# Kernel optimization log

Measured on AMD Instinct MI355X. Metric: run time of the kernel, lower is better.

## Reference

```python
import jax, jax.numpy as jnp
from jax import lax
import numpy as np

E = 3            # num_experts
HEAD_CONV = 128  # head_conv
N_HEADS = 3      # hm, wh, reg
HEAD_CH = 2      # channels per head
BN_EPS = 1e-5


def _conv(x, w, stride, pad, groups=1):
    return lax.conv_general_dilated(
        x, w, (stride, stride), [(pad, pad), (pad, pad)],
        feature_group_count=groups,
        dimension_numbers=('NCHW', 'OIHW', 'NCHW'))


def _maxpool3s2p1(x):
    return lax.reduce_window(
        x, -jnp.inf, lax.max, (1, 1, 3, 3), (1, 1, 2, 2),
        ((0, 0), (0, 0), (1, 1), (1, 1)))


def setup_inputs() -> dict:
    key = jax.random.key(0)
    ks = jax.random.split(key, 8)
    B, C, T, H, W = 16, 3, 5, 384, 384
    s = 0.05
    inp = {
        'x': jax.random.normal(ks[0], (B, C, T, H, W), jnp.float32),
        # gating network params
        'g_conv_w': jax.random.normal(ks[1], (64, C * T, 7, 7), jnp.float32) * s,
        'g_bn_gamma': jnp.ones((64,), jnp.float32),
        'g_bn_beta': jnp.zeros((64,), jnp.float32),
        'g_bn_mean': jnp.zeros((64,), jnp.float32),
        'g_bn_var': jnp.ones((64,), jnp.float32),
        'g_fc_w': jax.random.normal(ks[2], (E, 64), jnp.float32) * s,
        'g_fc_b': jnp.zeros((E,), jnp.float32),
        # frozen expert params (stacked over expert dim E)
        'e_conv1_w': jax.random.normal(ks[3], (E, 64, C * T, 7, 7), jnp.float32) * s,
        'e_conv1_b': jnp.zeros((E, 64), jnp.float32),
        'e_head_w1': jax.random.normal(ks[4], (E, N_HEADS * HEAD_CONV, 64, 3, 3), jnp.float32) * s,
        'e_head_b1': jnp.zeros((E, N_HEADS * HEAD_CONV), jnp.float32),
        'e_head_w2': jax.random.normal(ks[5], (E, N_HEADS * HEAD_CH, HEAD_CONV, 1, 1), jnp.float32) * s,
        'e_head_b2': jnp.zeros((E, N_HEADS * HEAD_CH), jnp.float32),
    }
    return inp


def reference(x, g_conv_w, g_bn_gamma, g_bn_beta, g_bn_mean, g_bn_var,
              g_fc_w, g_fc_b, e_conv1_w, e_conv1_b,
              e_head_w1, e_head_b1, e_head_w2, e_head_b2):
    b, c, t, h, w = x.shape
    xr = x.reshape(b, c * t, h, w)

    # ---- ConvGatingNetwork ----
    f = _conv(xr, g_conv_w, 2, 3)                                  # [B,64,H/2,W/2]
    inv = g_bn_gamma / jnp.sqrt(g_bn_var + BN_EPS)
    f = f * inv[None, :, None, None] + (g_bn_beta - g_bn_mean * inv)[None, :, None, None]
    f = jax.nn.relu(f)
    f = _maxpool3s2p1(f)                                           # [B,64,H/4,W/4]
    feat = f.mean(axis=(2, 3))                                     # [B,64]
    logits = feat @ g_fc_w.T + g_fc_b                              # [B,E]
    idx = jnp.argmax(logits, axis=1)                               # top-1
    onehot = jax.nn.one_hot(idx, E, dtype=logits.dtype)            # [B,E]
    density = onehot.mean(axis=0)
    density_proxy = jax.nn.softmax(logits, axis=1).mean(axis=0)
    aux_loss = (density * density_proxy).sum() * E

    # ---- Experts (frozen DSFNet stand-in), computed densely then gathered ----
    def expert(cw, cb, hw1, hb1, hw2, hb2):
        y = jax.nn.relu(_conv(xr, cw, 4, 3) + cb[None, :, None, None])       # [B,64,H/4,W/4]
        y = jax.nn.relu(_conv(y, hw1, 1, 1) + hb1[None, :, None, None])      # [B,384,h,w]
        y = _conv(y, hw2, 1, 0, groups=N_HEADS) + hb2[None, :, None, None]   # [B,6,h,w]
        return y

    out_all = jax.vmap(expert)(e_conv1_w, e_conv1_b, e_head_w1, e_head_b1,
                               e_head_w2, e_head_b2)               # [E,B,6,h,w]
    out_all = lax.stop_gradient(out_all)  # experts frozen + torch.no_grad
    out = jnp.einsum('be,ebchw->bchw', onehot, out_all)            # per-sample top-1 gather
    return out, 0.01 * aux_loss
```

## Files before the change

### kernel.cpp

```cpp
#include <hip/hip_runtime.h>
#include <math.h>

#define BB 16
#define CIN 15
#define HW 384
#define XPL 147456
#define NX 35389440
#define PH 96
#define GW 192
#define YP 98
#define Y1IPL (98*98*64)
#define OUT_ELEMS (BB*6*PH*PH)

#define OFF_WG   0
#define OFF_WE1  122880
#define OFF_WH   491520
#define OFF_GSH  1818624
#define OFF_FEAT 1818880
#define OFF_IDX  1822976
#define OFF_CBUF 2097152

typedef __attribute__((ext_vector_type(8))) short short8;
typedef __attribute__((ext_vector_type(4))) float floatx4;
typedef __attribute__((ext_vector_type(4))) unsigned int uintx4;
typedef __attribute__((ext_vector_type(2))) unsigned int uintx2;

__device__ __forceinline__ unsigned bf16rne(float f) {
  unsigned u = __float_as_uint(f);
  unsigned r = ((u >> 16) & 1u) + 0x7FFFu;
  return (u + r) >> 16;
}
__device__ __forceinline__ float bf2f(unsigned short s) {
  return __uint_as_float(((unsigned)s) << 16);
}

__global__ __launch_bounds__(256) void k_prep(
    const float* __restrict__ g_conv_w, const float* __restrict__ e_conv1_w,
    const float* __restrict__ e_head_w1,
    const float* __restrict__ gamma, const float* __restrict__ var,
    const float* __restrict__ beta,  const float* __restrict__ mean,
    unsigned char* __restrict__ wsb)
{
  int i = blockIdx.x * 256 + threadIdx.x;
  unsigned short* Wg  = (unsigned short*)(wsb + OFF_WG);
  unsigned short* We1 = (unsigned short*)(wsb + OFF_WE1);
  unsigned short* Wh  = (unsigned short*)(wsb + OFF_WH);
  float* gsh = (float*)(wsb + OFF_GSH);
  if (i < 61440) {
    int j = i & 7, lane = (i >> 3) & 63, mtc = i >> 9;
    int mt = mtc & 3, c = mtc >> 2, ic = c >> 1, h = c & 1;
    int oc = mt * 16 + (lane & 15), q = lane >> 4;
    int ky = 4 * h + q, kx = j;
    float v = 0.f;
    if (ky < 7 && kx < 7) v = g_conv_w[oc * 735 + ic * 49 + ky * 7 + kx];
    float inv = gamma[oc] * rsqrtf(var[oc] + 1e-5f);
    Wg[i] = (unsigned short)bf16rne(v * inv);
  } else if (i < 245760) {
    int r = i - 61440;
    int e = r / 61440, r2 = r % 61440;
    int j = r2 & 7, lane = (r2 >> 3) & 63, mtc = r2 >> 9;
    int mt = mtc & 3, c = mtc >> 2, ic = c >> 1, h = c & 1;
    int oc = mt * 16 + (lane & 15), q = lane >> 4;
    int ky = 4 * h + q, kx = j;
    float v = 0.f;
    if (ky < 7 && kx < 7) v = e_conv1_w[(e * 64 + oc) * 735 + ic * 49 + ky * 7 + kx];
    We1[r] = (unsigned short)bf16rne(v);
  } else if (i < 909312) {
    int r = i - 245760;
    int e = r / 221184, r2 = r % 221184;
    int j = r2 & 7, lane = (r2 >> 3) & 63, mtc = r2 >> 9;
    int mt = mtc % 24, chunk = mtc / 24;
    int kk = chunk >> 1, ih = chunk & 1;
    int oc = mt * 16 + (lane & 15), q = lane >> 4;
    int ic = ih * 32 + q * 8 + j;
    Wh[r] = (unsigned short)bf16rne(e_head_w1[((e * 384 + oc) * 64 + ic) * 9 + kk]);
  } else if (i < 909376) {
    int oc = i - 909312;
    float inv = gamma[oc] * rsqrtf(var[oc] + 1e-5f);
    gsh[oc] = beta[oc] - mean[oc] * inv;
  }
}

__global__ __launch_bounds__(256, 3) void k_gconv(
    const float* __restrict__ x, const unsigned short* __restrict__ Wg,
    const float* __restrict__ gsh, unsigned short* __restrict__ Cbuf)
{
  const int t = threadIdx.x, w = t >> 6, lane = t & 63, q = lane >> 4, ln = lane & 15;

  int lin = blockIdx.x + 12 * (blockIdx.y + 12 * blockIdx.z);
  int nl = (lin & 7) * 288 + (lin >> 3);
  const int b = nl / 144; int r144 = nl - b * 144;
  const int by = r144 / 12, bx = r144 - by * 12;

  const int px0 = bx * 16, py0 = by * 16;
  const int iy0 = 2 * py0 - 3, ix0 = 2 * px0 - 3;
  const bool edge = (bx == 0) | (bx == 11) | (by == 0) | (by == 11);
  const int xbase = b * CIN * XPL;

  __shared__ unsigned tilU[2][2280];

  const bool act = (t < 228);
  const int lic = t / 76, r2 = t - lic * 76, srow = r2 >> 1, half = r2 & 1;
  const int iy = iy0 + srow;
  const int A = ix0 + 20 * half - 1;
  const unsigned rowm = (iy >= 0 && iy < HW) ? 0xFFFFFFFFu : 0u;
  const int abase = xbase + iy * HW + A;
  const int dloc = (lic * 38 + srow) * 20 + 10 * half;

  floatx4 F[6];

  auto issue = [&](int c) {
    if (!act) return;
    int a = abase + (c * 3 + lic) * XPL;
    if (!edge) {
      const float* src = x + a;
#pragma unroll
      for (int s = 0; s < 6; ++s) F[s] = *(const floatx4*)(src + 4 * s);
    } else {
#pragma unroll
      for (int s = 0; s < 6; ++s) {
        int as = a + 4 * s;
        as = max(as, 0); as = min(as, NX - 4);
        F[s] = *(const floatx4*)(x + as);
      }
    }
  };

  auto commit = [&](unsigned* buf) {
    if (!act) return;
    float f[24];
#pragma unroll
    for (int s = 0; s < 6; ++s) {
      f[4*s] = F[s].x; f[4*s+1] = F[s].y; f[4*s+2] = F[s].z; f[4*s+3] = F[s].w;
    }
    unsigned* dst = buf + dloc;
    if (!edge) {
#pragma unroll
      for (int jj = 0; jj < 5; ++jj) {
        uintx2 pr;
        pr.x = bf16rne(f[1 + 4*jj]) | (bf16rne(f[2 + 4*jj]) << 16);
        pr.y = bf16rne(f[3 + 4*jj]) | (bf16rne(f[4 + 4*jj]) << 16);
        *(uintx2*)(dst + 2 * jj) = pr;
      }
    } else {
#pragma unroll
      for (int jj = 0; jj < 5; ++jj) {
        uintx2 pr;
#pragma unroll
        for (int k = 0; k < 2; ++k) {
          int j = 2 * jj + k;
          int cc = A + 1 + 2 * j;
          unsigned m = rowm;
          m &= ((cc >= 0) && (cc < HW)) ? 0xFFFFFFFFu : 0xFFFF0000u;
          m &= ((cc + 1 >= 0) && (cc + 1 < HW)) ? 0xFFFFFFFFu : 0x0000FFFFu;
          unsigned d = (bf16rne(f[1 + 2*j]) | (bf16rne(f[2 + 2*j]) << 16)) & m;
          if (k == 0) pr.x = d; else pr.y = d;
        }
        *(uintx2*)(dst + 2 * jj) = pr;
      }
    }
  };

  floatx4 acc[4][4];
#pragma unroll
  for (int mt = 0; mt < 4; ++mt)
#pragma unroll
    for (int nt = 0; nt < 4; ++nt) acc[mt][nt] = 0.f;

  issue(0);
  commit(tilU[0]);
  __syncthreads();

#pragma unroll 1
  for (int c = 0; c < 5; ++c) {
    if (c < 4) issue(c + 1);
    const unsigned* buf = tilU[c & 1];
#pragma unroll
    for (int l2 = 0; l2 < 3; ++l2) {
      const int ic = c * 3 + l2;
#pragma unroll
      for (int h = 0; h < 2; ++h) {
        short8 af[4];
#pragma unroll
        for (int mt = 0; mt < 4; ++mt)
          af[mt] = *(const short8*)(Wg + (((ic * 2 + h) * 4 + mt) << 9) + lane * 8);
        short8 bfv[4];
#pragma unroll
        for (int nt = 0; nt < 4; ++nt) {
          int rrow = 2 * (w * 4 + nt) + 4 * h + q;
          int bd = l2 * 760 + rrow * 20 + ln;
          union { unsigned u[4]; short8 s; } cv;
          cv.u[0] = buf[bd]; cv.u[1] = buf[bd + 1];
          cv.u[2] = buf[bd + 2]; cv.u[3] = buf[bd + 3];
          bfv[nt] = cv.s;
        }
#pragma unroll
        for (int mt = 0; mt < 4; ++mt)
#pragma unroll
          for (int nt = 0; nt < 4; ++nt)
            acc[mt][nt] = __builtin_amdgcn_mfma_f32_16x16x32_bf16(af[mt], bfv[nt], acc[mt][nt], 0, 0, 0);
      }
    }
    if (c < 4) commit(tilU[(c + 1) & 1]);
    __syncthreads();
  }

#pragma unroll
  for (int nt = 0; nt < 4; ++nt) {
    int py = py0 + w * 4 + nt, px = px0 + ln;
    size_t rowo = (((size_t)b * GW + py) * GW + px) * 64;
#pragma unroll
    for (int mt = 0; mt < 4; ++mt) {
      int ocb = mt * 16 + q * 4;
      float v0 = fmaxf(acc[mt][nt][0] + gsh[ocb + 0], 0.f);
      float v1 = fmaxf(acc[mt][nt][1] + gsh[ocb + 1], 0.f);
      float v2 = fmaxf(acc[mt][nt][2] + gsh[ocb + 2], 0.f);
      float v3 = fmaxf(acc[mt][nt][3] + gsh[ocb + 3], 0.f);
      uintx2 pr;
      pr.x = (bf16rne(v1) << 16) | bf16rne(v0);
      pr.y = (bf16rne(v3) << 16) | bf16rne(v2);
      *(uintx2*)(Cbuf + rowo + ocb) = pr;
    }
  }
}

__global__ __launch_bounds__(256) void k_pool(const unsigned short* __restrict__ Cb,
                                              float* __restrict__ feat)
{
  const int py = blockIdx.x, b = blockIdx.y;
  const int t = threadIdx.x, oc = t & 63, strip = t >> 6;
  const unsigned short* base = Cb + (size_t)b * GW * GW * 64 + oc;
  float sum = 0.f;
  for (int px = strip * 24; px < strip * 24 + 24; ++px) {
    float m = 0.f;
#pragma unroll
    for (int dy = 0; dy < 3; ++dy) {
      int row = 2 * py - 1 + dy;
      if (row < 0 || row >= GW) continue;
#pragma unroll
      for (int dx = 0; dx < 3; ++dx) {
        int col = 2 * px - 1 + dx;
        if (col < 0 || col >= GW) continue;
        m = fmaxf(m, bf2f(base[((size_t)row * GW + col) * 64]));
      }
    }
    sum += m;
  }
  __shared__ float red[4][64];
  red[strip][oc] = sum;
  __syncthreads();
  if (t < 64) {
    float s = red[0][oc] + red[1][oc] + red[2][oc] + red[3][oc];
    atomicAdd(&feat[b * 64 + oc], s);
  }
}

__global__ __launch_bounds__(64) void k_gate_fc(
    const float* __restrict__ feat, const float* __restrict__ fcw,
    const float* __restrict__ fcb, int* __restrict__ idxb,
    float* __restrict__ out_aux)
{
  __shared__ float sm[16][3];
  __shared__ int sidx[16];
  int t = threadIdx.x;
  if (t < 16) {
    float l[3];
#pragma unroll
    for (int e = 0; e < 3; ++e) {
      float s = fcb[e];
      for (int c = 0; c < 64; ++c)
        s = fmaf(feat[t * 64 + c] * (1.f / 9216.f), fcw[e * 64 + c], s);
      l[e] = s;
    }
    int best = 0; float bv = l[0];
    if (l[1] > bv) { bv = l[1]; best = 1; }
    if (l[2] > bv) { bv = l[2]; best = 2; }
    sidx[t] = best; idxb[t] = best;
    float mx = fmaxf(l[0], fmaxf(l[1], l[2]));
    float e0 = expf(l[0] - mx), e1 = expf(l[1] - mx), e2 = expf(l[2] - mx);
    float d = e0 + e1 + e2;
    sm[t][0] = e0 / d; sm[t][1] = e1 / d; sm[t][2] = e2 / d;
  }
  __syncthreads();
  if (t == 0) {
    float aux = 0.f;
    for (int e = 0; e < 3; ++e) {
      float cnt = 0.f, pr = 0.f;
      for (int b = 0; b < 16; ++b) { cnt += (sidx[b] == e) ? 1.f : 0.f; pr += sm[b][e]; }
      aux += (cnt / 16.f) * (pr / 16.f);
    }
    *out_aux = 0.01f * aux * 3.f;
  }
}

__global__ __launch_bounds__(256) void k_zring(unsigned short* __restrict__ Y1)
{
  const int b = blockIdx.x, t = threadIdx.x;
  uintx4* Yv = (uintx4*)Y1;
  uintx4 z = 0;
  for (int i = t; i < 3104; i += 256) {
    int v;
    if (i < 784) {
      v = (b * YP + 0) * 784 + i;
    } else if (i < 1568) {
      v = (b * YP + 97) * 784 + (i - 784);
    } else {
      int j = i - 1568;
      int colg = j / 768;
      int jj = j - colg * 768;
      int col = colg ? 97 : 0;
      int rr = 1 + (jj >> 3);
      v = (b * YP + rr) * 784 + col * 8 + (jj & 7);
    }
    Yv[v] = z;
  }
}

__global__ __launch_bounds__(256, 4) void k_econv(
    const float* __restrict__ x, const unsigned short* __restrict__ We1,
    const float* __restrict__ biasp, const int* __restrict__ idxb,
    unsigned short* __restrict__ Y1)
{
  const int t = threadIdx.x, w = t >> 6, lane = t & 63, q = lane >> 4, ln = lane & 15;
  const int b = blockIdx.z;
  const int e = idxb[b];
  const unsigned short* W = We1 + e * 61440;
  const float* bs = biasp + e * 64;
  const int px0 = blockIdx.x * 16, py0 = blockIdx.y * 8;
  const int px = px0 + ln;

  const int c0 = 4 * px - 3;
  const int acol = c0 - 1;
  unsigned pm[4];
#pragma unroll
  for (int j = 0; j < 4; ++j) {
    int t0 = 2 * j, t1 = 2 * j + 1;
    unsigned m0 = (c0 + t0 >= 0 && c0 + t0 < HW) ? 0x0000FFFFu : 0u;
    unsigned m1 = (c0 + t1 >= 0 && c0 + t1 < HW) ? 0xFFFF0000u : 0u;
    pm[j] = m0 | m1;
  }

  int syq[2];
#pragma unroll
  for (int nt = 0; nt < 2; ++nt) syq[nt] = 4 * (py0 + w * 2 + nt) + q - 3;
  const int xbase = b * CIN * XPL;

  floatx4 acc[4][2];
#pragma unroll
  for (int mt = 0; mt < 4; ++mt)
#pragma unroll
    for (int nt = 0; nt < 2; ++nt) acc[mt][nt] = 0.f;

#pragma unroll 3
  for (int ic = 0; ic < CIN; ++ic) {
    const int icb = xbase + ic * XPL;
#pragma unroll
    for (int h = 0; h < 2; ++h) {
      short8 af[4];
#pragma unroll
      for (int mt = 0; mt < 4; ++mt)
        af[mt] = *(const short8*)(W + (((ic * 2 + h) * 4 + mt) << 9) + lane * 8);
      short8 bf[2];
#pragma unroll
      for (int nt = 0; nt < 2; ++nt) {
        int iy = syq[nt] + 4 * h;
        bool rv = (iy >= 0) && (iy < HW) && ((4 * h + q) < 7);
        int a0 = icb + iy * HW + acol;
        a0 = max(a0, 0); a0 = min(a0, NX - 12);
        const float* fp = x + a0;
        floatx4 fA = *(const floatx4*)(fp);
        floatx4 fB = *(const floatx4*)(fp + 4);
        floatx4 fC = *(const floatx4*)(fp + 8);
        float g[8];
        g[0] = fA.y; g[1] = fA.z; g[2] = fA.w; g[3] = fB.x;
        g[4] = fB.y; g[5] = fB.z; g[6] = fB.w; g[7] = fC.x;
        union { unsigned u[4]; short8 s; } cv;
#pragma unroll
        for (int j = 0; j < 4; ++j) {
          unsigned p = __builtin_amdgcn_perm(__float_as_uint(g[2 * j + 1]),
                                             __float_as_uint(g[2 * j]), 0x07060302u);
          p &= pm[j];
          cv.u[j] = rv ? p : 0u;
        }
        bf[nt] = cv.s;
      }
#pragma unroll
      for (int mt = 0; mt < 4; ++mt)
#pragma unroll
        for (int nt = 0; nt < 2; ++nt)
          acc[mt][nt] = __builtin_amdgcn_mfma_f32_16x16x32_bf16(af[mt], bf[nt], acc[mt][nt], 0, 0, 0);
    }
  }

#pragma unroll
  for (int nt = 0; nt < 2; ++nt) {
    int py = py0 + w * 2 + nt;
    size_t rowo = (((size_t)b * YP + py + 1) * YP + px + 1) * 64;
#pragma unroll
    for (int mt = 0; mt < 4; ++mt) {
      int ocb = mt * 16 + q * 4;
      float v0 = fmaxf(acc[mt][nt][0] + bs[ocb + 0], 0.f);
      float v1 = fmaxf(acc[mt][nt][1] + bs[ocb + 1], 0.f);
      float v2 = fmaxf(acc[mt][nt][2] + bs[ocb + 2], 0.f);
      float v3 = fmaxf(acc[mt][nt][3] + bs[ocb + 3], 0.f);
      uintx2 pr;
      pr.x = (bf16rne(v1) << 16) | bf16rne(v0);
      pr.y = (bf16rne(v3) << 16) | bf16rne(v2);
      *(uintx2*)(Y1 + rowo + ocb) = pr;
    }
  }
}

__global__ __launch_bounds__(768, 3) void k_headm(
    const unsigned short* __restrict__ Y1, const unsigned short* __restrict__ Whp,
    const float* __restrict__ b1, const float* __restrict__ w2,
    const float* __restrict__ b2, const int* __restrict__ idxb,
    float* __restrict__ out)
{
  const int t = threadIdx.x, w = t >> 6, lane = t & 63, q = lane >> 4, ln = lane & 15;
  const int wo = w & 3, wn = w >> 2;
  const int b = blockIdx.z, px0 = blockIdx.x * 16, py0 = blockIdx.y * 6;
  const int e = idxb[b];
  const unsigned short* W = Whp + e * 221184;

  __shared__ unsigned short patch[8 * 18 * 72];
  __shared__ float sred[6][4][16][6];

  {
    uintx4 vv[2];
#pragma unroll
    for (int r = 0; r < 2; ++r) {
      int i = r * 768 + t;
      if (i < 1152) {
        int row = i / 144, rem = i % 144, col = rem >> 3, s = rem & 7;
        vv[r] = *(const uintx4*)(Y1 + (((size_t)b * YP + py0 + row) * YP + (px0 + col)) * 64 + s * 8);
      }
    }
#pragma unroll
    for (int r = 0; r < 2; ++r) {
      int i = r * 768 + t;
      if (i < 1152) {
        int row = i / 144, rem = i % 144, col = rem >> 3, s = rem & 7;
        *(uintx4*)(patch + (row * 18 + col) * 72 + s * 8) = vv[r];
      }
    }
  }
  __syncthreads();

  floatx4 acc[6][2];
#pragma unroll
  for (int mt = 0; mt < 6; ++mt)
#pragma unroll
    for (int j = 0; j < 2; ++j) acc[mt][j] = 0.f;

#pragma unroll
  for (int kk = 0; kk < 9; ++kk) {
    const int ky = kk / 3, kx = kk % 3;
#pragma unroll
    for (int ih = 0; ih < 2; ++ih) {
      short8 bf[2];
#pragma unroll
      for (int j = 0; j < 2; ++j) {
        int nt = wn * 2 + j;
        int off = ((nt + ky) * 18 + (ln + kx)) * 72 + ih * 32 + q * 8;
        bf[j] = *(const short8*)(patch + off);
      }
      const int cbase = ((kk * 2 + ih) * 24 + wo * 6) << 9;
#pragma unroll
      for (int mt = 0; mt < 6; ++mt) {
        short8 af = *(const short8*)(W + cbase + (mt << 9) + lane * 8);
#pragma unroll
        for (int j = 0; j < 2; ++j)
          acc[mt][j] = __builtin_amdgcn_mfma_f32_16x16x32_bf16(af, bf[j], acc[mt][j], 0, 0, 0);
      }
    }
  }

#pragma unroll
  for (int j = 0; j < 2; ++j) {
    const int nt = wn * 2 + j;
    float part[6] = {0.f, 0.f, 0.f, 0.f, 0.f, 0.f};
#pragma unroll
    for (int mt = 0; mt < 6; ++mt) {
      int ocb = wo * 96 + mt * 16 + q * 4;
#pragma unroll
      for (int r = 0; r < 4; ++r) {
        int oc = ocb + r;
        float y = fmaxf(acc[mt][j][r] + b1[e * 384 + oc], 0.f);
        int g = oc >> 7, kb = oc & 127;
        part[2 * g]     += y * w2[(e * 6 + 2 * g) * 128 + kb];
        part[2 * g + 1] += y * w2[(e * 6 + 2 * g + 1) * 128 + kb];
      }
    }
#pragma unroll
    for (int c = 0; c < 6; ++c) {
      part[c] += __shfl_down(part[c], 32);
      part[c] += __shfl_down(part[c], 16);
    }
    if (q == 0) {
#pragma unroll
      for (int c = 0; c < 6; ++c) sred[nt][wo][ln][c] = part[c];
    }
  }
  __syncthreads();
  if (t < 576) {
    int pix = t / 6, c = t % 6;
    int nt = pix >> 4, pl = pix & 15;
    float s = sred[nt][0][pl][c] + sred[nt][1][pl][c] + sred[nt][2][pl][c] +
              sred[nt][3][pl][c] + b2[e * 6 + c];
    out[(((size_t)(b * 6 + c)) * PH + (py0 + nt)) * PH + (px0 + pl)] = s;
  }
}

extern "C" void kernel_launch(void* const* d_in, const int* in_sizes, int n_in,
                              void* d_out, int out_size, void* d_ws, size_t ws_size,
                              hipStream_t stream)
{
  const float* x         = (const float*)d_in[0];
  const float* g_fc_w    = (const float*)d_in[6];
  const float* g_fc_b    = (const float*)d_in[7];
  const float* e_conv1_b = (const float*)d_in[9];
  const float* e_head_b1 = (const float*)d_in[11];
  const float* e_head_w2 = (const float*)d_in[12];
  const float* e_head_b2 = (const float*)d_in[13];

  unsigned char* wsb = (unsigned char*)d_ws;
  unsigned short* Wg  = (unsigned short*)(wsb + OFF_WG);
  unsigned short* We1 = (unsigned short*)(wsb + OFF_WE1);
  unsigned short* Wh  = (unsigned short*)(wsb + OFF_WH);
  float* gsh  = (float*)(wsb + OFF_GSH);
  float* feat = (float*)(wsb + OFF_FEAT);
  int*   idxb = (int*)(wsb + OFF_IDX);
  unsigned short* Cbuf = (unsigned short*)(wsb + OFF_CBUF);
  unsigned short* Y1   = (unsigned short*)(wsb + OFF_CBUF);

  float* out = (float*)d_out;
  float* out_aux = out + OUT_ELEMS;

  hipMemsetAsync(feat, 0, 16 * 64 * sizeof(float), stream);
  hipLaunchKernelGGL(k_prep, dim3(3553), dim3(256), 0, stream,
                     (const float*)d_in[1], (const float*)d_in[8], (const float*)d_in[10],
                     (const float*)d_in[2], (const float*)d_in[5],
                     (const float*)d_in[3], (const float*)d_in[4], wsb);

  hipLaunchKernelGGL(k_gconv, dim3(12, 12, 16), dim3(256), 0, stream,
                     x, Wg, gsh, Cbuf);
  hipLaunchKernelGGL(k_pool, dim3(96, 16), dim3(256), 0, stream, Cbuf, feat);
  hipLaunchKernelGGL(k_gate_fc, dim3(1), dim3(64), 0, stream,
                     feat, g_fc_w, g_fc_b, idxb, out_aux);

  hipLaunchKernelGGL(k_zring, dim3(16), dim3(256), 0, stream, Y1);
  hipLaunchKernelGGL(k_econv, dim3(6, 12, 16), dim3(256), 0, stream,
                     x, We1, e_conv1_b, idxb, Y1);

  hipLaunchKernelGGL(k_headm, dim3(6, 16, 16), dim3(768), 0, stream,
                     Y1, Wh, e_head_b1, e_head_w2, e_head_b2, idxb, out);
}
```

Measured before the change: 595.5 us.

## Stage expert conv1 input tile in LDS with double-buffered register prefetch

The expert stride-4 7x7 conv kernel used to read overlapping input rows straight from global memory, with per-lane bounds masks. It now loads a 35x35 bf16-packed input patch per channel group (3 channels at a time) into shared memory. Loads for the next group go through registers and overlap the MFMA work on the current buffer. This cuts redundant global loads and per-element masking, at the cost of LDS usage, barriers, more registers and lower launch-bounds occupancy (4 to 3).

After: 599.0 us. About the same (+0.6%).

```diff
diff --git a/kernel.cpp b/kernel.cpp
--- a/kernel.cpp
+++ b/kernel.cpp
@@ -316,7 +316,7 @@
   }
 }
 
-__global__ __launch_bounds__(256, 4) void k_econv(
+__global__ __launch_bounds__(256, 3) void k_econv(
     const float* __restrict__ x, const unsigned short* __restrict__ We1,
     const float* __restrict__ biasp, const int* __restrict__ idxb,
     unsigned short* __restrict__ Y1)
@@ -328,22 +328,84 @@
   const float* bs = biasp + e * 64;
   const int px0 = blockIdx.x * 16, py0 = blockIdx.y * 8;
   const int px = px0 + ln;
-
-  const int c0 = 4 * px - 3;
-  const int acol = c0 - 1;
-  unsigned pm[4];
-#pragma unroll
-  for (int j = 0; j < 4; ++j) {
-    int t0 = 2 * j, t1 = 2 * j + 1;
-    unsigned m0 = (c0 + t0 >= 0 && c0 + t0 < HW) ? 0x0000FFFFu : 0u;
-    unsigned m1 = (c0 + t1 >= 0 && c0 + t1 < HW) ? 0xFFFF0000u : 0u;
-    pm[j] = m0 | m1;
-  }
-
-  int syq[2];
-#pragma unroll
-  for (int nt = 0; nt < 2; ++nt) syq[nt] = 4 * (py0 + w * 2 + nt) + q - 3;
-  const int xbase = b * CIN * XPL;
+  const bool edge = (blockIdx.x == 0) | (blockIdx.y == 0);
+  const bool lmask = (blockIdx.x == 0);
+
+  __shared__ unsigned xt[2][3710];
+
+  const bool act = (t < 210);
+  const int icl = act ? (t / 70) : 0;
+  const int r2 = t - icl * 70;
+  const int srow = (r2 >> 1) % 35, half = r2 & 1;
+  const int iy = 4 * py0 - 3 + srow;
+  const int colbase = half ? (4 * px0 + 32) : (4 * px0 - 4);
+  const int abase = b * CIN * XPL + iy * HW + colbase;
+  const int dloc = (icl * 35 + srow) * 35 + (half ? 18 : 0);
+
+  if (t < 35) { xt[0][3675 + t] = 0u; xt[1][3675 + t] = 0u; }
+
+  floatx4 F[10];
+
+  auto issue = [&](int c) {
+    if (!act) return;
+    int a = abase + (c * 3 + icl) * XPL;
+    if (!edge) {
+      const float* src = x + a;
+      if (!half) {
+#pragma unroll
+        for (int s = 0; s < 10; ++s) F[s] = *(const floatx4*)(src + 4 * s);
+      } else {
+#pragma unroll
+        for (int s = 0; s < 8; ++s) F[s] = *(const floatx4*)(src + 4 * s);
+      }
+    } else {
+      const int n = half ? 8 : 10;
+#pragma unroll
+      for (int s = 0; s < 10; ++s) {
+        if (s < n) {
+          int as = a + 4 * s;
+          as = max(as, 0); as = min(as, NX - 4);
+          F[s] = *(const floatx4*)(x + as);
+        }
+      }
+    }
+  };
+
+  auto commit = [&](unsigned* buf) {
+    if (!act) return;
+    unsigned* dst = buf + dloc;
+    if (iy < 0) {
+      if (!half) {
+#pragma unroll
+        for (int k = 0; k < 18; ++k) dst[k] = 0;
+      } else {
+#pragma unroll
+        for (int k = 0; k < 16; ++k) dst[k] = 0;
+      }
+      return;
+    }
+    if (!half) {
+#pragma unroll
+      for (int k = 0; k < 18; ++k) {
+        unsigned lo = __float_as_uint(F[(1 + 2 * k) >> 2][(1 + 2 * k) & 3]);
+        unsigned hi = __float_as_uint(F[(2 + 2 * k) >> 2][(2 + 2 * k) & 3]);
+        unsigned u = __builtin_amdgcn_perm(hi, lo, 0x07060302u);
+        if (lmask) {
+          if (k == 0) u = 0u;
+          else if (k == 1) u &= 0xFFFF0000u;
+        }
+        dst[k] = u;
+      }
+    } else {
+#pragma unroll
+      for (int k = 0; k < 16; ++k) {
+        unsigned lo = __float_as_uint(F[(1 + 2 * k) >> 2][(1 + 2 * k) & 3]);
+        unsigned hi = (k == 15) ? 0u
+                                : __float_as_uint(F[(2 + 2 * k) >> 2][(2 + 2 * k) & 3]);
+        dst[k] = __builtin_amdgcn_perm(hi, lo, 0x07060302u);
+      }
+    }
+  };
 
   floatx4 acc[4][2];
 #pragma unroll
@@ -351,45 +413,42 @@
 #pragma unroll
     for (int nt = 0; nt < 2; ++nt) acc[mt][nt] = 0.f;
 
-#pragma unroll 3
-  for (int ic = 0; ic < CIN; ++ic) {
-    const int icb = xbase + ic * XPL;
-#pragma unroll
-    for (int h = 0; h < 2; ++h) {
-      short8 af[4];
-#pragma unroll
-      for (int mt = 0; mt < 4; ++mt)
-        af[mt] = *(const short8*)(W + (((ic * 2 + h) * 4 + mt) << 9) + lane * 8);
-      short8 bf[2];
-#pragma unroll
-      for (int nt = 0; nt < 2; ++nt) {
-        int iy = syq[nt] + 4 * h;
-        bool rv = (iy >= 0) && (iy < HW) && ((4 * h + q) < 7);
-        int a0 = icb + iy * HW + acol;
-        a0 = max(a0, 0); a0 = min(a0, NX - 12);
-        const float* fp = x + a0;
-        floatx4 fA = *(const floatx4*)(fp);
-        floatx4 fB = *(const floatx4*)(fp + 4);
-        floatx4 fC = *(const floatx4*)(fp + 8);
-        float g[8];
-        g[0] = fA.y; g[1] = fA.z; g[2] = fA.w; g[3] = fB.x;
-        g[4] = fB.y; g[5] = fB.z; g[6] = fB.w; g[7] = fC.x;
-        union { unsigned u[4]; short8 s; } cv;
-#pragma unroll
-        for (int j = 0; j < 4; ++j) {
-          unsigned p = __builtin_amdgcn_perm(__float_as_uint(g[2 * j + 1]),
-                                             __float_as_uint(g[2 * j]), 0x07060302u);
-          p &= pm[j];
-          cv.u[j] = rv ? p : 0u;
+  issue(0);
+  commit(xt[0]);
+  __syncthreads();
+
+#pragma unroll 1
+  for (int c = 0; c < 5; ++c) {
+    if (c < 4) issue(c + 1);
+    const unsigned* buf = xt[c & 1];
+#pragma unroll
+    for (int l2 = 0; l2 < 3; ++l2) {
+      const int ic = c * 3 + l2;
+#pragma unroll
+      for (int h = 0; h < 2; ++h) {
+        short8 af[4];
+#pragma unroll
+        for (int mt = 0; mt < 4; ++mt)
+          af[mt] = *(const short8*)(W + (((ic * 2 + h) * 4 + mt) << 9) + lane * 8);
+        short8 bf[2];
+#pragma unroll
+        for (int nt = 0; nt < 2; ++nt) {
+          int lr = 4 * (2 * w + nt) + 4 * h + q;
+          int bd = (l2 * 35 + lr) * 35 + 2 * ln;
+          union { unsigned u[4]; short8 s; } cv;
+          cv.u[0] = buf[bd]; cv.u[1] = buf[bd + 1];
+          cv.u[2] = buf[bd + 2]; cv.u[3] = buf[bd + 3];
+          bf[nt] = cv.s;
         }
-        bf[nt] = cv.s;
-      }
-#pragma unroll
-      for (int mt = 0; mt < 4; ++mt)
-#pragma unroll
-        for (int nt = 0; nt < 2; ++nt)
-          acc[mt][nt] = __builtin_amdgcn_mfma_f32_16x16x32_bf16(af[mt], bf[nt], acc[mt][nt], 0, 0, 0);
-    }
+#pragma unroll
+        for (int mt = 0; mt < 4; ++mt)
+#pragma unroll
+          for (int nt = 0; nt < 2; ++nt)
+            acc[mt][nt] = __builtin_amdgcn_mfma_f32_16x16x32_bf16(af[mt], bf[nt], acc[mt][nt], 0, 0, 0);
+      }
+    }
+    if (c < 4) commit(xt[(c + 1) & 1]);
+    __syncthreads();
   }
 
 #pragma unroll
```
